# Kernel optimization log

Hardware: AMD Instinct MI355X
Metric: run time of the kernel (lower is better)

Reference implementation:

```python
import jax, jax.numpy as jnp
import numpy as np

B, T, C = 2, 2048, 1024
H = 16
DK = C // H


def setup_inputs() -> dict:
    key = jax.random.key(0)
    ks = jax.random.split(key, 5)
    x = jax.random.normal(ks[0], (B, T, C), dtype=jnp.float32)
    # causal mask, broadcastable to [B, H, T, T]; mask==0 -> -inf
    mask = jnp.tril(jnp.ones((T, T), dtype=jnp.int32))[None, None]
    s = 1.0 / np.sqrt(C)
    qkv_w = jax.random.normal(ks[1], (3 * C, C), dtype=jnp.float32) * s  # torch Linear layout [out,in]
    qkv_b = jnp.zeros((3 * C,), dtype=jnp.float32)
    out_w = jax.random.normal(ks[2], (C, C), dtype=jnp.float32) * s
    out_b = jnp.zeros((C,), dtype=jnp.float32)
    return {"x": x, "mask": mask, "qkv_w": qkv_w, "qkv_b": qkv_b,
            "out_w": out_w, "out_b": out_b}


def reference(x, mask, qkv_w, qkv_b, out_w, out_b):
    b, t, c = x.shape
    qkv = x @ qkv_w.T + qkv_b                       # [B,T,3C]
    qkv = qkv.reshape(b, t, 3, H, DK)
    q, k, v = qkv[:, :, 0], qkv[:, :, 1], qkv[:, :, 2]   # [B,T,H,DK]
    scores = jnp.einsum('bqhd,bkhd->bhqk', q, k) / np.sqrt(DK)
    scores = jnp.where(mask == 0, -jnp.inf, scores)
    attn_weights = jax.nn.softmax(scores, axis=-1)       # [B,H,T,T]
    attn_out = jnp.einsum('bhqk,bkhd->bqhd', attn_weights, v).reshape(b, t, c)
    out = attn_out @ out_w.T + out_b
    return out, attn_weights
```

## Files before the change

kernel.cpp:

```cpp
#include <hip/hip_runtime.h>
#include <hip/hip_bf16.h>

typedef short short8  __attribute__((ext_vector_type(8)));
typedef short short4v __attribute__((ext_vector_type(4)));
typedef __bf16 bf16x8 __attribute__((ext_vector_type(8)));
typedef float f32x4   __attribute__((ext_vector_type(4)));

__device__ __forceinline__ void mfma16(f32x4& d, short8 a, short8 b) {
    d = __builtin_amdgcn_mfma_f32_16x16x32_bf16(
            __builtin_bit_cast(bf16x8, a), __builtin_bit_cast(bf16x8, b), d, 0, 0, 0);
}

__device__ __forceinline__ unsigned short f2bf(float f) {
    union { float f; unsigned u; } a; a.f = f;
    unsigned u = a.u;
    return (unsigned short)((u + 0x7fffu + ((u >> 16) & 1u)) >> 16);
}
__device__ __forceinline__ float bf2f(unsigned short us) {
    union { unsigned u; float f; } a; a.u = ((unsigned)us) << 16;
    return a.f;
}

__global__ void cvt_all(const float* __restrict__ x, const float* __restrict__ w1,
                        const float* __restrict__ w2,
                        unsigned short* __restrict__ ox, unsigned short* __restrict__ o1,
                        unsigned short* __restrict__ o2) {
    int i = blockIdx.x * 256 + threadIdx.x;
    const float* src; unsigned short* dst; int j;
    if (i < 1048576)      { src = x;  dst = ox; j = i; }
    else if (i < 1835008) { src = w1; dst = o1; j = i - 1048576; }
    else                  { src = w2; dst = o2; j = i - 1835008; }
    float4 v = ((const float4*)src)[j];
    ushort4 o;
    o.x = f2bf(v.x); o.y = f2bf(v.y); o.z = f2bf(v.z); o.w = f2bf(v.w);
    ((ushort4*)dst)[j] = o;
}

template<int OUTBF, int VTF, int BM, int BN, int MAP>
__global__ __launch_bounds__(256)
void gemm_bt(const unsigned short* __restrict__ A, const unsigned short* __restrict__ Bw,
             const float* __restrict__ bias, void* __restrict__ Cout,
             unsigned short* __restrict__ vt, unsigned short* __restrict__ khb,
             int M, int N, int K)
{
    constexpr int MM = BM / 32;
    constexpr int NN = BN / 32;
    __shared__ unsigned short As[BM * 64];
    __shared__ unsigned short Bs[BN * 64];

    const int tid  = threadIdx.x;
    const int lane = tid & 63;
    const int wid  = tid >> 6;

    int row0, col0;
    if constexpr (MAP == 1) {
        const int xcd = blockIdx.x & 7, lid = blockIdx.x >> 3;
        const int super = lid / 24, sub = lid % 24;
        row0 = ((super << 3) + (sub & 7)) << 7;
        col0 = (xcd * 3 + (sub >> 3)) << 7;
    } else {
        const int xcd = blockIdx.x & 7, lid = blockIdx.x >> 3;
        row0 = (lid >> 1) << 6;
        col0 = ((xcd << 1) + (lid & 1)) << 6;
    }
    const int wr = (wid >> 1) * (BM >> 1);
    const int wc = (wid & 1) * (BN >> 1);
    const int rl = lane & 15;
    const int g  = lane >> 4;

    f32x4 acc[MM][NN] = {};

    for (int k0 = 0; k0 < K; k0 += 64) {
        __syncthreads();
#pragma unroll
        for (int rd = 0; rd < (BM >> 5); ++rd) {
            int s  = rd * 256 + tid;
            int r  = s >> 3, cs = s & 7;
            int cg = cs ^ (r & 7);
            __builtin_amdgcn_global_load_lds(
                (__attribute__((address_space(1))) void*)(A + (size_t)(row0 + r) * K + k0 + cg * 8),
                (__attribute__((address_space(3))) void*)(As + s * 8), 16, 0, 0);
        }
#pragma unroll
        for (int rd = 0; rd < (BN >> 5); ++rd) {
            int s  = rd * 256 + tid;
            int r  = s >> 3, cs = s & 7;
            int cg = cs ^ (r & 7);
            __builtin_amdgcn_global_load_lds(
                (__attribute__((address_space(1))) void*)(Bw + (size_t)(col0 + r) * K + k0 + cg * 8),
                (__attribute__((address_space(3))) void*)(Bs + s * 8), 16, 0, 0);
        }
        __syncthreads();

#pragma unroll
        for (int h = 0; h < 2; ++h) {
            short8 af[MM], bf[NN];
#pragma unroll
            for (int m = 0; m < MM; ++m) {
                int rr = wr + m * 16 + rl;
                int ch = ((h << 2) + g) ^ (rr & 7);
                af[m] = *(const short8*)(As + rr * 64 + ch * 8);
            }
#pragma unroll
            for (int n = 0; n < NN; ++n) {
                int rr = wc + n * 16 + rl;
                int ch = ((h << 2) + g) ^ (rr & 7);
                bf[n] = *(const short8*)(Bs + rr * 64 + ch * 8);
            }
#pragma unroll
            for (int m = 0; m < MM; ++m)
#pragma unroll
                for (int n = 0; n < NN; ++n)
                    mfma16(acc[m][n], af[m], bf[n]);
        }
    }

    const int b  = row0 >> 11;
    const int tg = (row0 & 2047) + wr + (g << 2);
#pragma unroll
    for (int n = 0; n < NN; ++n) {
        int col = col0 + wc + n * 16 + rl;
        float bv = bias[col];
        if (VTF && col >= 2048) {
            int hd = col - 2048;
            unsigned short* vr = vt + ((size_t)((b << 4) + (hd >> 6)) * 64 + (hd & 63)) * 2048;
#pragma unroll
            for (int m = 0; m < MM; ++m) {
                short4v p;
#pragma unroll
                for (int r = 0; r < 4; ++r) p[r] = (short)f2bf(acc[m][n][r] + bv);
                *(short4v*)(vr + tg + m * 16) = p;
            }
        } else if (VTF && col >= 1024) {
            int hd = col - 1024;
            unsigned short* kr = khb + ((size_t)((b << 4) + (hd >> 6)) << 17) + (hd & 63);
#pragma unroll
            for (int m = 0; m < MM; ++m)
#pragma unroll
                for (int r = 0; r < 4; ++r)
                    kr[(size_t)(tg + m * 16 + r) << 6] = f2bf(acc[m][n][r] + bv);
        } else if (VTF) {
#pragma unroll
            for (int m = 0; m < MM; ++m)
#pragma unroll
                for (int r = 0; r < 4; ++r)
                    ((unsigned short*)Cout)[(size_t)(row0 + wr + m * 16 + (g << 2) + r) * 1024 + col]
                        = f2bf(acc[m][n][r] + bv);
        } else {
#pragma unroll
            for (int m = 0; m < MM; ++m) {
#pragma unroll
                for (int r = 0; r < 4; ++r) {
                    int row = row0 + wr + m * 16 + (g << 2) + r;
                    float v = acc[m][n][r] + bv;
                    if (OUTBF) ((unsigned short*)Cout)[(size_t)row * N + col] = f2bf(v);
                    else       ((float*)Cout)[(size_t)row * N + col] = v;
                }
            }
        }
    }
}

__device__ __forceinline__ int S_addr(int row, int col) {
    return (row << 11) + ((((col >> 3) ^ (row & 7))) << 3) + (col & 7);
}

__global__ __launch_bounds__(256, 2)
void attn_kernel(const unsigned short* __restrict__ qbuf,
                 const unsigned short* __restrict__ khb,
                 const unsigned short* __restrict__ vt,
                 float* __restrict__ wout,
                 unsigned short* __restrict__ aout)
{
    __shared__ unsigned short Ss[16 * 2048];
    __shared__ float part[4][16];

    const int bid = (int)(((blockIdx.x & 7) << 9) + (blockIdx.x >> 3));
    const int qt = bid & 127;
    const int bh = bid >> 7;
    const int b = bh >> 4, h = bh & 15;
    const int q0 = qt << 4;
    const int tid = threadIdx.x;
    const int wid = tid >> 6;
    const int lane = tid & 63;
    const int rl = lane & 15;
    const int g  = lane >> 4;

    int nt = (qt + 4) & ~3;
    if (nt > 128) nt = 128;
    const int ntiles = nt;
    const int KPAD = ntiles << 4;

    const unsigned short* Qb = qbuf + (size_t)((b << 11) + q0) * 1024 + (h << 6);
    short8 qf0 = *(const short8*)(Qb + rl * 1024 + g * 8);
    short8 qf1 = *(const short8*)(Qb + rl * 1024 + 32 + g * 8);

    const unsigned short* Kh = khb + ((size_t)bh << 17);

    float psum[4] = {0.f, 0.f, 0.f, 0.f};

    {
        short8 ka0, ka1, kb0, kb1;
        {
            const unsigned short* kp = Kh + (size_t)((wid * 16 + rl) << 6);
            ka0 = *(const short8*)(kp + g * 8);
            ka1 = *(const short8*)(kp + 32 + g * 8);
        }
        if (wid + 4 < ntiles) {
            const unsigned short* kp = Kh + (size_t)((((wid + 4) * 16) + rl) << 6);
            kb0 = *(const short8*)(kp + g * 8);
            kb1 = *(const short8*)(kp + 32 + g * 8);
        } else { kb0 = ka0; kb1 = ka1; }
        for (int kt = wid; kt < ntiles; kt += 4) {
            short8 kc0 = ka0, kc1 = ka1;
            ka0 = kb0; ka1 = kb1;
            if (kt + 8 < ntiles) {
                const unsigned short* kp2 = Kh + (size_t)((((kt + 8) * 16) + rl) << 6);
                kb0 = *(const short8*)(kp2 + g * 8);
                kb1 = *(const short8*)(kp2 + 32 + g * 8);
            }
            f32x4 acc = {};
            __builtin_amdgcn_s_setprio(1);
            mfma16(acc, qf0, kc0);
            mfma16(acc, qf1, kc1);
            __builtin_amdgcn_s_setprio(0);
            int col = kt * 16 + rl;
#pragma unroll
            for (int r = 0; r < 4; ++r) {
                int qrow = g * 4 + r;
                float e = (col <= q0 + qrow) ? __expf(acc[r] * 0.125f) : 0.0f;
                Ss[S_addr(qrow, col)] = f2bf(e);
                psum[r] += e;
            }
        }
    }
#pragma unroll
    for (int m = 8; m; m >>= 1)
#pragma unroll
        for (int r = 0; r < 4; ++r) psum[r] += __shfl_xor(psum[r], m);
    if (rl == 0) {
#pragma unroll
        for (int r = 0; r < 4; ++r) part[wid][g * 4 + r] = psum[r];
    }
    __syncthreads();

    f32x4 p0 = {}, p1 = {};
    const unsigned short* vrow = vt + ((size_t)(bh << 6) + wid * 16 + rl) * 2048;
    const int np = KPAD >> 6;
    const int wrow = wid + (g << 2);
    const float invw = 1.0f / (part[0][wrow] + part[1][wrow] + part[2][wrow] + part[3][wrow]);
    float* worow = wout + ((size_t)bh * 2048 + q0 + wrow) * 2048;
    short8 bv0 = *(const short8*)(vrow + (g << 3));
    short8 bv1 = *(const short8*)(vrow + 32 + (g << 3));
    for (int ic = 0; ic < 32; ++ic) {
        int colb = (ic << 6) + (rl << 2);
        f32x4 o;
        if (ic < np) {
            short8 c0 = bv0, c1 = bv1;
            if (ic + 1 < np) {
                bv0 = *(const short8*)(vrow + ((ic + 1) << 6) + (g << 3));
                bv1 = *(const short8*)(vrow + ((ic + 1) << 6) + 32 + (g << 3));
            }
            int k0c = (ic << 3) + g;
            short8 a0 = *(const short8*)(Ss + (rl << 11) + ((k0c ^ (rl & 7)) << 3));
            short8 a1 = *(const short8*)(Ss + (rl << 11) + (((k0c + 4) ^ (rl & 7)) << 3));
            __builtin_amdgcn_s_setprio(1);
            mfma16(p0, a0, c0);
            mfma16(p1, a1, c1);
            __builtin_amdgcn_s_setprio(0);
            short4v sv = *(const short4v*)(Ss + S_addr(wrow, colb));
            o[0] = bf2f((unsigned short)sv[0]) * invw;
            o[1] = bf2f((unsigned short)sv[1]) * invw;
            o[2] = bf2f((unsigned short)sv[2]) * invw;
            o[3] = bf2f((unsigned short)sv[3]) * invw;
        } else {
            o[0] = 0.f; o[1] = 0.f; o[2] = 0.f; o[3] = 0.f;
        }
        __builtin_nontemporal_store(o, (f32x4*)(worow + colb));
    }

    f32x4 pacc = p0 + p1;
#pragma unroll
    for (int r = 0; r < 4; ++r) {
        int qrow = g * 4 + r;
        float inv = 1.0f / (part[0][qrow] + part[1][qrow] + part[2][qrow] + part[3][qrow]);
        float v = pacc[r] * inv;
        aout[(size_t)((b << 11) + q0 + qrow) * 1024 + (h << 6) + wid * 16 + rl] = f2bf(v);
    }
}

extern "C" void kernel_launch(void* const* d_in, const int* in_sizes, int n_in,
                              void* d_out, int out_size, void* d_ws, size_t ws_size,
                              hipStream_t stream)
{
    const float* x     = (const float*)d_in[0];
    const float* qkv_w = (const float*)d_in[2];
    const float* qkv_b = (const float*)d_in[3];
    const float* out_w = (const float*)d_in[4];
    const float* out_b = (const float*)d_in[5];

    char* ws = (char*)d_ws;
    unsigned short* xbf   = (unsigned short*)(ws);
    unsigned short* wqkv  = (unsigned short*)(ws + 8388608);
    unsigned short* woutw = (unsigned short*)(ws + 14680064);
    unsigned short* qbuf  = (unsigned short*)(ws + 16777216);
    unsigned short* vt    = (unsigned short*)(ws + 25165824);
    unsigned short* aout  = (unsigned short*)(ws + 33554432);
    unsigned short* khb   = (unsigned short*)(ws + 41943040);

    float* out  = (float*)d_out;
    float* wout = (float*)d_out + 4194304;

    cvt_all<<<8192, 256, 0, stream>>>(x, qkv_w, out_w, xbf, wqkv, woutw);

    gemm_bt<1, 1, 128, 128, 1><<<768, 256, 0, stream>>>(xbf, wqkv, qkv_b, qbuf, vt, khb, 4096, 3072, 1024);
    attn_kernel<<<4096, 256, 0, stream>>>(qbuf, khb, vt, wout, aout);
    gemm_bt<0, 0, 64, 64, 2><<<1024, 256, 0, stream>>>(aout, woutw, out_b, out, nullptr, nullptr, 4096, 1024, 1024);
}
```

Baseline: 211.6 us.

## Use eight waves per attention block, splitting key tiles and PV chunks

Doubles the attention block to 512 threads. The score/exp phase strides key tiles across eight waves. The P·V phase splits key chunks by parity between two four-wave groups, which are then combined through a new shared-memory partial buffer and an extra barrier. The aim is more waves per CU to hide memory latency and raise store throughput on the large attention-weight output, at the cost of an added LDS reduction, an extra sync, and narrower 8-byte weight stores per lane.

```diff
diff --git a/kernel.cpp b/kernel.cpp
--- a/kernel.cpp
+++ b/kernel.cpp
@@ -5,6 +5,7 @@
 typedef short short4v __attribute__((ext_vector_type(4)));
 typedef __bf16 bf16x8 __attribute__((ext_vector_type(8)));
 typedef float f32x4   __attribute__((ext_vector_type(4)));
+typedef float f32x2   __attribute__((ext_vector_type(2)));
 
 __device__ __forceinline__ void mfma16(f32x4& d, short8 a, short8 b) {
     d = __builtin_amdgcn_mfma_f32_16x16x32_bf16(
@@ -165,7 +166,7 @@
     return (row << 11) + ((((col >> 3) ^ (row & 7))) << 3) + (col & 7);
 }
 
-__global__ __launch_bounds__(256, 2)
+__global__ __launch_bounds__(512, 2)
 void attn_kernel(const unsigned short* __restrict__ qbuf,
                  const unsigned short* __restrict__ khb,
                  const unsigned short* __restrict__ vt,
@@ -173,7 +174,8 @@
                  unsigned short* __restrict__ aout)
 {
     __shared__ unsigned short Ss[16 * 2048];
-    __shared__ float part[4][16];
+    __shared__ float part[8][16];
+    __shared__ float pp[4][16][16];
 
     const int bid = (int)(((blockIdx.x & 7) << 9) + (blockIdx.x >> 3));
     const int qt = bid & 127;
@@ -190,6 +192,7 @@
     if (nt > 128) nt = 128;
     const int ntiles = nt;
     const int KPAD = ntiles << 4;
+    const int np = KPAD >> 6;
 
     const unsigned short* Qb = qbuf + (size_t)((b << 11) + q0) * 1024 + (h << 6);
     short8 qf0 = *(const short8*)(Qb + rl * 1024 + g * 8);
@@ -206,16 +209,16 @@
             ka0 = *(const short8*)(kp + g * 8);
             ka1 = *(const short8*)(kp + 32 + g * 8);
         }
-        if (wid + 4 < ntiles) {
-            const unsigned short* kp = Kh + (size_t)((((wid + 4) * 16) + rl) << 6);
-            kb0 = *(const short8*)(kp + g * 8);
-            kb1 = *(const short8*)(kp + 32 + g * 8);
-        } else { kb0 = ka0; kb1 = ka1; }
-        for (int kt = wid; kt < ntiles; kt += 4) {
+        {
+            const unsigned short* kp2 = Kh + (size_t)((((wid + 8) * 16) + rl) << 6);
+            kb0 = *(const short8*)(kp2 + g * 8);
+            kb1 = *(const short8*)(kp2 + 32 + g * 8);
+        }
+        for (int kt = wid; kt < ntiles; kt += 8) {
             short8 kc0 = ka0, kc1 = ka1;
             ka0 = kb0; ka1 = kb1;
-            if (kt + 8 < ntiles) {
-                const unsigned short* kp2 = Kh + (size_t)((((kt + 8) * 16) + rl) << 6);
+            if (kt + 16 < ntiles) {
+                const unsigned short* kp2 = Kh + (size_t)((((kt + 16) * 16) + rl) << 6);
                 kb0 = *(const short8*)(kp2 + g * 8);
                 kb1 = *(const short8*)(kp2 + 32 + g * 8);
             }
@@ -244,22 +247,27 @@
     }
     __syncthreads();
 
+    const int dt = (wid & 3) << 4;
+    const int ph = wid >> 2;
     f32x4 p0 = {}, p1 = {};
-    const unsigned short* vrow = vt + ((size_t)(bh << 6) + wid * 16 + rl) * 2048;
-    const int np = KPAD >> 6;
-    const int wrow = wid + (g << 2);
-    const float invw = 1.0f / (part[0][wrow] + part[1][wrow] + part[2][wrow] + part[3][wrow]);
-    float* worow = wout + ((size_t)bh * 2048 + q0 + wrow) * 2048;
-    short8 bv0 = *(const short8*)(vrow + (g << 3));
-    short8 bv1 = *(const short8*)(vrow + 32 + (g << 3));
+    const unsigned short* vrow = vt + ((size_t)(bh << 6) + dt + rl) * 2048;
+    const int srow = tid >> 5;
+    const int scol = (tid & 31) << 1;
+    const float invw = 1.0f / (part[0][srow] + part[1][srow] + part[2][srow] + part[3][srow]
+                             + part[4][srow] + part[5][srow] + part[6][srow] + part[7][srow]);
+    float* worow = wout + ((size_t)bh * 2048 + q0 + srow) * 2048;
+    int jc = ph;
+    short8 bv0, bv1;
+    if (jc < np) {
+        bv0 = *(const short8*)(vrow + (jc << 6) + (g << 3));
+        bv1 = *(const short8*)(vrow + (jc << 6) + 32 + (g << 3));
+    }
     for (int ic = 0; ic < 32; ++ic) {
-        int colb = (ic << 6) + (rl << 2);
-        f32x4 o;
-        if (ic < np) {
+        if (ic == jc && ic < np) {
             short8 c0 = bv0, c1 = bv1;
-            if (ic + 1 < np) {
-                bv0 = *(const short8*)(vrow + ((ic + 1) << 6) + (g << 3));
-                bv1 = *(const short8*)(vrow + ((ic + 1) << 6) + 32 + (g << 3));
+            if (jc + 2 < np) {
+                bv0 = *(const short8*)(vrow + ((jc + 2) << 6) + (g << 3));
+                bv1 = *(const short8*)(vrow + ((jc + 2) << 6) + 32 + (g << 3));
             }
             int k0c = (ic << 3) + g;
             short8 a0 = *(const short8*)(Ss + (rl << 11) + ((k0c ^ (rl & 7)) << 3));
@@ -268,24 +276,34 @@
             mfma16(p0, a0, c0);
             mfma16(p1, a1, c1);
             __builtin_amdgcn_s_setprio(0);
-            short4v sv = *(const short4v*)(Ss + S_addr(wrow, colb));
-            o[0] = bf2f((unsigned short)sv[0]) * invw;
-            o[1] = bf2f((unsigned short)sv[1]) * invw;
-            o[2] = bf2f((unsigned short)sv[2]) * invw;
-            o[3] = bf2f((unsigned short)sv[3]) * invw;
+            jc += 2;
+        }
+        f32x2 o;
+        if (ic < np) {
+            unsigned sv = *(const unsigned*)(Ss + S_addr(srow, (ic << 6) + scol));
+            o[0] = bf2f((unsigned short)(sv & 0xffffu)) * invw;
+            o[1] = bf2f((unsigned short)(sv >> 16)) * invw;
         } else {
-            o[0] = 0.f; o[1] = 0.f; o[2] = 0.f; o[3] = 0.f;
-        }
-        __builtin_nontemporal_store(o, (f32x4*)(worow + colb));
+            o[0] = 0.f; o[1] = 0.f;
+        }
+        __builtin_nontemporal_store(o, (f32x2*)(worow + (ic << 6) + scol));
     }
 
     f32x4 pacc = p0 + p1;
-#pragma unroll
-    for (int r = 0; r < 4; ++r) {
-        int qrow = g * 4 + r;
-        float inv = 1.0f / (part[0][qrow] + part[1][qrow] + part[2][qrow] + part[3][qrow]);
-        float v = pacc[r] * inv;
-        aout[(size_t)((b << 11) + q0 + qrow) * 1024 + (h << 6) + wid * 16 + rl] = f2bf(v);
+    if (wid >= 4) {
+#pragma unroll
+        for (int r = 0; r < 4; ++r) pp[wid - 4][g * 4 + r][rl] = pacc[r];
+    }
+    __syncthreads();
+    if (wid < 4) {
+#pragma unroll
+        for (int r = 0; r < 4; ++r) {
+            int qrow = g * 4 + r;
+            float inv = 1.0f / (part[0][qrow] + part[1][qrow] + part[2][qrow] + part[3][qrow]
+                              + part[4][qrow] + part[5][qrow] + part[6][qrow] + part[7][qrow]);
+            float v = (pacc[r] + pp[wid][qrow][rl]) * inv;
+            aout[(size_t)((b << 11) + q0 + qrow) * 1024 + (h << 6) + dt + rl] = f2bf(v);
+        }
     }
 }
 
@@ -314,6 +332,6 @@
     cvt_all<<<8192, 256, 0, stream>>>(x, qkv_w, out_w, xbf, wqkv, woutw);
 
     gemm_bt<1, 1, 128, 128, 1><<<768, 256, 0, stream>>>(xbf, wqkv, qkv_b, qbuf, vt, khb, 4096, 3072, 1024);
-    attn_kernel<<<4096, 256, 0, stream>>>(qbuf, khb, vt, wout, aout);
+    attn_kernel<<<4096, 512, 0, stream>>>(qbuf, khb, vt, wout, aout);
     gemm_bt<0, 0, 64, 64, 2><<<1024, 256, 0, stream>>>(aout, woutw, out_b, out, nullptr, nullptr, 4096, 1024, 1024);
 }
```

After: 224.5 us. +6.1%, slower.
